# Kernel tuning notes

Measured on AMD Instinct MI355X. Metric: run time of the kernel, lower is better.

Reference implementation:

```python
import jax, jax.numpy as jnp
import numpy as np

# Module hyperparameters (from init_kwargs)
M = 2049          # NpointsMesh (odd)
TAU = 3e-6        # Gaussian spreading width
XLIMS = (0.0, 1.0)
MU0 = 1.0
L = abs(XLIMS[1] - XLIMS[0])
TWO_PI = 2.0 * np.pi
B, N = 16, 512


def _grids():
    kGrid = jnp.asarray(np.linspace(-(M // 2), M // 2, M), jnp.float32)
    xGrid = jnp.asarray(TWO_PI * np.linspace(XLIMS[0], XLIMS[1], M + 1)[:-1] / L, jnp.float32)
    return kGrid, xGrid


def setup_inputs() -> dict:
    key = jax.random.key(0)
    kx, = jax.random.split(key, 1)
    x = jax.random.uniform(kx, (B, N), dtype=jnp.float32)  # points inside xLims
    kGrid, _ = _grids()
    multRe0 = (4.0 * np.pi / (kGrid ** 2 + MU0 ** 2))[None, :].astype(jnp.float32)
    multRe1 = (4.0 * np.pi / (kGrid ** 2 + 1.0))[None, :].astype(jnp.float32)
    zeros = jnp.zeros((1, M), jnp.float32)
    return {"x": x, "multRe0": multRe0, "multIm0": zeros,
            "multRe1": multRe1, "multIm1": zeros}


def reference(x, multRe0, multIm0, multRe1, multIm1):
    kGrid, xGrid = _grids()
    # Gaussian spreading: (B, N, M)
    diff = x[..., None] * (TWO_PI / L) - xGrid
    g = jnp.exp(-(diff * diff) / (4.0 * TAU))
    red = jnp.sum(g, axis=1)  # (B, M)
    # NOTE: tf.signal.fftshift/ifftshift default to ALL axes; jnp matches that default.
    fftG = jnp.fft.fftshift(jnp.fft.fft(jax.lax.complex(red, jnp.zeros_like(red)))) * (L / TWO_PI)
    deconv = jnp.sqrt(np.pi / TAU) * jnp.exp((kGrid ** 2) * TAU)  # (M,) real
    rfft = fftG * deconv
    Re, Im = jnp.real(rfft), jnp.imag(rfft)

    def mix(mRe, mIm):
        # Faithful to source (incl. its naming quirk): real = mRe*Re - mRe*Im,
        # imag = mIm*Re + mIm*Im
        return jax.lax.complex(mRe * Re - mRe * Im, mIm * Re + mIm * Im)

    multFFT = jnp.stack([mix(multRe0, multIm0), mix(multRe1, multIm1)], axis=1)  # (B, 2, M)
    multDeconv = multFFT * deconv  # broadcast over (B, 2, M)
    irfft = jnp.real(jnp.fft.ifft(jnp.fft.ifftshift(multDeconv)))  # (B, 2, M)
    # local = irfft[:,None,:,:] * g[:,:,None,:]; fmm = sum over mesh / M  -> einsum
    fmm = jnp.einsum('bnm,bcm->bnc', g, irfft) / M  # (B, N, 2)
    return fmm
```

## Files before the change

### kernel.cpp

```cpp
#include <hip/hip_runtime.h>
#include <math.h>

#define MM 2049
#define BB 16
#define NN 512
#define JH 1025
#define JP 1040
#define SZ 8
#define PCH 128
#define JCH 5
#define CT2 205
#define TCH2 5

static constexpr double D_TWO_PI    = 6.283185307179586476925286766559;
static constexpr double D_STEP      = D_TWO_PI / 2049.0;
static constexpr float  F_TWO_PI    = 6.28318530717958647692f;
static constexpr float  INV_4TAU    = 83333.33333333333f;
static constexpr float  PI_OVER_TAU = 1047197.5511965977f;
static constexpr float  TWO_TAU     = 6.0e-6f;
static constexpr float  INV_2PI     = 0.15915494309189533f;
static constexpr float  INV_M       = 1.0f / 2049.0f;
static constexpr float  WINF        = 8.0f;


__global__ void k_sdft1(const float* __restrict__ x, float2* __restrict__ PSp,
                        float* __restrict__ out) {
    __shared__ float  LA[PCH];
    __shared__ float  LB[PCH];
    __shared__ float2 SD[PCH];
    __shared__ float  Lz;
    const int b  = blockIdx.y;
    const int z  = blockIdx.z;
    const int a0 = 1 + PCH * z;
    const int b0 = 2049 - PCH * (z + 1);
    if (blockIdx.x == 0 && z == 0) {
        for (int i = threadIdx.x; i < NN * 2; i += 256) out[b * NN * 2 + i] = 0.0f;
    }
    for (int i = threadIdx.x; i < PCH; i += 256) { LA[i] = 0.0f; LB[i] = 0.0f; }
    if (threadIdx.x == 0) Lz = 0.0f;
    __syncthreads();
    for (int n = threadIdx.x; n < NN; n += 256) {
        float xv = x[b * NN + n];
        float xa = xv * F_TWO_PI;
        float p  = xv * (float)MM;
        int m0 = (int)ceilf(p - WINF);  if (m0 < 0) m0 = 0;
        int m1 = (int)floorf(p + WINF); if (m1 > MM - 1) m1 = MM - 1;
        bool hitA = (m1 >= a0) && (m0 <= a0 + PCH - 1);
        bool hitB = (m1 >= b0) && (m0 <= b0 + PCH - 1);
        bool hit0 = (z == 0) && (m0 == 0);
        if (!(hitA || hitB || hit0)) continue;
        for (int m = m0; m <= m1; ++m) {
            float xg = (float)((double)m * D_STEP);
            float d  = xa - xg;
            float g  = expf(-(d * d) * INV_4TAU);
            unsigned ia = (unsigned)(m - a0);
            unsigned ib = (unsigned)(m - b0);
            if (ia < PCH) atomicAdd(&LA[ia], g);
            if (ib < PCH) atomicAdd(&LB[ib], g);
            if (hit0 && m == 0) atomicAdd(&Lz, g);
        }
    }
    __syncthreads();
    for (int i = threadIdx.x; i < PCH; i += 256) {
        float ra = LA[i], rb = LB[PCH - 1 - i];
        SD[i] = make_float2(ra + rb, ra - rb);
    }
    __syncthreads();
    const int j = blockIdx.x * 256 + threadIdx.x;
    if (j >= JH) return;
    float ct, st;
    { float ang = (float)((double)j * D_STEP); __sincosf(ang, &st, &ct); }
    float c, s;
    { int r0 = (j * a0) % MM; float ph = (float)((double)r0 * D_STEP); __sincosf(ph, &s, &c); }
    float accc = 0.0f, accs = 0.0f;
    #pragma unroll 4
    for (int i = 0; i < PCH; ++i) {
        float2 sd = SD[i];
        accc = fmaf(sd.x, c, accc);
        accs = fmaf(sd.y, s, accs);
        float t1 = s * st, t2 = s * ct;
        float cn = fmaf(c, ct, -t1);
        float sn = fmaf(c, st,  t2);
        c = cn; s = sn;
    }
    if (z == 0) accc += Lz;
    PSp[((size_t)b * SZ + z) * JP + j] = make_float2(accc, accs);
}

__global__ __launch_bounds__(256)
void k_dft2g(const float2* __restrict__ PSp,
             const float* __restrict__ mRe0, const float* __restrict__ mIm0,
             const float* __restrict__ mRe1, const float* __restrict__ mIm1,
             const float* __restrict__ x, float* __restrict__ out) {
    __shared__ float4 lab[JH];
    __shared__ float2 irfL[CT2];
    __shared__ float2 irfH[CT2];
    const int tc  = blockIdx.x;
    const int b   = blockIdx.y;
    const int t0  = tc * CT2;
    const int tid = threadIdx.x;

    for (int i = tid; i < JH; i += 256) {
        const int j = i;
        float cs = 0.0f, sn = 0.0f;
        const float2* base = PSp + (size_t)b * SZ * JP + j;
        #pragma unroll
        for (int z = 0; z < SZ; ++z) {
            float2 ps = base[(size_t)z * JP];
            cs += ps.x; sn += ps.y;
        }
        const int msh = j + 1024;
        const float jf = (float)j;
        const float d2 = PI_OVER_TAU * expf(jf * jf * TWO_TAU);
        const float fac = (j == 0) ? 1.0f : 2.0f;
        const float sc = INV_2PI * d2 * fac;
        float4 v;
        v.x =  sc * mRe1[msh] * cs;
        v.y =  sc * mRe0[msh] * cs;
        v.z = -sc * mIm1[msh] * sn;
        v.w = -sc * mIm0[msh] * sn;
        lab[i] = v;
    }
    __syncthreads();

    if (tid < CT2) {
        const int t = t0 + tid;
        float ct, st;
        { float ang = (float)((double)t * D_STEP); __sincosf(ang, &st, &ct); }
        float E0 = 0.0f, O0 = 0.0f, E1 = 0.0f, O1 = 0.0f;
        for (int q0 = 0; q0 < JH; q0 += 128) {
            const int qe = min(q0 + 128, JH);
            float c, s;
            { int r0 = (t * q0) % MM; float ph = (float)((double)r0 * D_STEP); __sincosf(ph, &s, &c); }
            #pragma unroll 4
            for (int i = q0; i < qe; ++i) {
                float4 v = lab[i];
                E0 = fmaf(v.x, c, E0);
                O0 = fmaf(v.z, s, O0);
                E1 = fmaf(v.y, c, E1);
                O1 = fmaf(v.w, s, O1);
                float t1 = s * st, t2 = s * ct;
                float cn = fmaf(c, ct, -t1);
                float sn2 = fmaf(c, st,  t2);
                c = cn; s = sn2;
            }
        }
        irfL[tid] = make_float2((E0 - O0) * INV_M, (E1 - O1) * INV_M);
        irfH[tid] = make_float2((E0 + O0) * INV_M, (E1 + O1) * INV_M);
    }
    __syncthreads();

    const int L0 = t0, L1 = t0 + CT2 - 1;
    const int H0 = MM - L1, H1 = MM - max(t0, 1);
    for (int n = tid; n < NN; n += 256) {
        const int p = b * NN + n;
        float xv = x[p];
        float xa = xv * F_TWO_PI;
        float pp = xv * (float)MM;
        int m0 = (int)ceilf(pp - WINF);  if (m0 < 0) m0 = 0;
        int m1 = (int)floorf(pp + WINF); if (m1 > MM - 1) m1 = MM - 1;
        float a0 = 0.0f, a1 = 0.0f;
        int lo = max(m0, L0), hi = min(m1, L1);
        for (int m = lo; m <= hi; ++m) {
            float xg = (float)((double)m * D_STEP);
            float d  = xa - xg;
            float g  = expf(-(d * d) * INV_4TAU);
            float2 v = irfL[m - L0];
            a0 = fmaf(g, v.x, a0);
            a1 = fmaf(g, v.y, a1);
        }
        int lo2 = max(m0, H0), hi2 = min(m1, H1);
        for (int m = lo2; m <= hi2; ++m) {
            float xg = (float)((double)m * D_STEP);
            float d  = xa - xg;
            float g  = expf(-(d * d) * INV_4TAU);
            float2 v = irfH[(MM - m) - t0];
            a0 = fmaf(g, v.x, a0);
            a1 = fmaf(g, v.y, a1);
        }
        if ((hi >= lo) || (hi2 >= lo2)) {
            atomicAdd(&out[p * 2 + 0], a0 * INV_M);
            atomicAdd(&out[p * 2 + 1], a1 * INV_M);
        }
    }
}

extern "C" void kernel_launch(void* const* d_in, const int* in_sizes, int n_in,
                              void* d_out, int out_size, void* d_ws, size_t ws_size,
                              hipStream_t stream) {
    const float* x    = (const float*)d_in[0];
    const float* mRe0 = (const float*)d_in[1];
    const float* mIm0 = (const float*)d_in[2];
    const float* mRe1 = (const float*)d_in[3];
    const float* mIm1 = (const float*)d_in[4];
    float* out = (float*)d_out;

    float2* PSp = (float2*)d_ws;

    k_sdft1<<<dim3(JCH, BB, SZ), 256, 0, stream>>>(x, PSp, out);
    k_dft2g<<<dim3(TCH2, BB), 256, 0, stream>>>(PSp, mRe0, mIm0, mRe1, mIm1, x, out);
}
```

Baseline: 106.2 us.

## Split inverse DFT over j across 16 lanes with shuffle reduction and more blocks

The second kernel now computes 16 output frequencies per block instead of 205. Each frequency's sum over j is split across 16 lanes of 65 terms each and combined with xor shuffles. The grid grows from 80 to 1040 blocks, which removes the long serial per-thread loop of 1025 twiddle steps and the idle threads in each block. In exchange, every block recomputes the 1025-entry lab table and rescans all 512 points for the gather, which adds redundant work and more atomics on the output.

```diff
diff --git a/kernel.cpp b/kernel.cpp
--- a/kernel.cpp
+++ b/kernel.cpp
@@ -9,8 +9,10 @@
 #define SZ 8
 #define PCH 128
 #define JCH 5
-#define CT2 205
-#define TCH2 5
+#define TB 16
+#define JS 16
+#define JSL 65
+#define NTC 65
 
 static constexpr double D_TWO_PI    = 6.283185307179586476925286766559;
 static constexpr double D_STEP      = D_TWO_PI / 2049.0;
@@ -93,11 +95,11 @@
              const float* __restrict__ mRe1, const float* __restrict__ mIm1,
              const float* __restrict__ x, float* __restrict__ out) {
     __shared__ float4 lab[JH];
-    __shared__ float2 irfL[CT2];
-    __shared__ float2 irfH[CT2];
+    __shared__ float2 irfL[TB];
+    __shared__ float2 irfH[TB];
     const int tc  = blockIdx.x;
     const int b   = blockIdx.y;
-    const int t0  = tc * CT2;
+    const int t0  = tc * TB;
     const int tid = threadIdx.x;
 
     for (int i = tid; i < JH; i += 256) {
@@ -123,34 +125,45 @@
     }
     __syncthreads();
 
-    if (tid < CT2) {
-        const int t = t0 + tid;
+    {
+        const int q  = tid & (JS - 1);
+        const int tt = tid >> 4;
+        const int t  = t0 + tt;
+        const int j0 = q * JSL;
+        const int j1 = min(j0 + JSL, JH);
         float ct, st;
         { float ang = (float)((double)t * D_STEP); __sincosf(ang, &st, &ct); }
+        float c, s;
+        { int r0 = (t * j0) % MM; float ph = (float)((double)r0 * D_STEP); __sincosf(ph, &s, &c); }
         float E0 = 0.0f, O0 = 0.0f, E1 = 0.0f, O1 = 0.0f;
-        for (int q0 = 0; q0 < JH; q0 += 128) {
-            const int qe = min(q0 + 128, JH);
-            float c, s;
-            { int r0 = (t * q0) % MM; float ph = (float)((double)r0 * D_STEP); __sincosf(ph, &s, &c); }
-            #pragma unroll 4
-            for (int i = q0; i < qe; ++i) {
-                float4 v = lab[i];
-                E0 = fmaf(v.x, c, E0);
-                O0 = fmaf(v.z, s, O0);
-                E1 = fmaf(v.y, c, E1);
-                O1 = fmaf(v.w, s, O1);
-                float t1 = s * st, t2 = s * ct;
-                float cn = fmaf(c, ct, -t1);
-                float sn2 = fmaf(c, st,  t2);
-                c = cn; s = sn2;
-            }
-        }
-        irfL[tid] = make_float2((E0 - O0) * INV_M, (E1 - O1) * INV_M);
-        irfH[tid] = make_float2((E0 + O0) * INV_M, (E1 + O1) * INV_M);
-    }
-    __syncthreads();
-
-    const int L0 = t0, L1 = t0 + CT2 - 1;
+        #pragma unroll 4
+        for (int i = j0; i < j1; ++i) {
+            float4 v = lab[i];
+            E0 = fmaf(v.x, c, E0);
+            O0 = fmaf(v.z, s, O0);
+            E1 = fmaf(v.y, c, E1);
+            O1 = fmaf(v.w, s, O1);
+            float t1 = s * st, t2 = s * ct;
+            float cn = fmaf(c, ct, -t1);
+            float sn2 = fmaf(c, st,  t2);
+            c = cn; s = sn2;
+        }
+        #pragma unroll
+        for (int off = 8; off > 0; off >>= 1) {
+            E0 += __shfl_xor(E0, off);
+            O0 += __shfl_xor(O0, off);
+            E1 += __shfl_xor(E1, off);
+            O1 += __shfl_xor(O1, off);
+        }
+        if (q == 0 && t < JH) {
+            irfL[tt] = make_float2((E0 - O0) * INV_M, (E1 - O1) * INV_M);
+            irfH[tt] = make_float2((E0 + O0) * INV_M, (E1 + O1) * INV_M);
+        }
+    }
+    __syncthreads();
+
+    const int L1 = min(t0 + TB, JH) - 1;
+    const int L0 = t0;
     const int H0 = MM - L1, H1 = MM - max(t0, 1);
     for (int n = tid; n < NN; n += 256) {
         const int p = b * NN + n;
@@ -198,5 +211,5 @@
     float2* PSp = (float2*)d_ws;
 
     k_sdft1<<<dim3(JCH, BB, SZ), 256, 0, stream>>>(x, PSp, out);
-    k_dft2g<<<dim3(TCH2, BB), 256, 0, stream>>>(PSp, mRe0, mIm0, mRe1, mIm1, x, out);
+    k_dft2g<<<dim3(NTC, BB), 256, 0, stream>>>(PSp, mRe0, mIm0, mRe1, mIm1, x, out);
 }
```

Measured after the change: 91.01 us. 1.17x faster.
